# Kernel optimization log

Measured on AMD Instinct MI355X. Metric: run time of the kernel, lower is better.

Reference implementation:

```python
import jax, jax.numpy as jnp
import numpy as np

EPS_NORM = 1e-12  # torch F.normalize eps
EPS_SUM = 1e-8
NEG_BIG = -1e9    # mask value for softmax (sims/temp is bounded by 10)


def setup_inputs() -> dict:
    key = jax.random.key(0)
    k1, k2 = jax.random.split(key)
    B, R, D = 128, 4096, 256
    reps = jax.random.normal(k1, (B, R, D), dtype=jnp.float32)
    query_rels = jax.random.randint(k2, (B,), 0, R, dtype=jnp.int64)
    # learned scalar params (per __init__ defaults: thr_init=0.8, strength_init=0.05)
    threshold_raw = jnp.asarray(0.8 * 2.0 - 1.0, dtype=jnp.float32)
    strength_raw = jnp.asarray(0.05 * 5.0 - 1.0, dtype=jnp.float32)
    weight_scale = jnp.asarray(1.0, dtype=jnp.float32)
    temperature = jnp.asarray(1.0, dtype=jnp.float32)
    return {
        "final_relation_representations": reps,
        "query_rels": query_rels,
        "threshold_raw": threshold_raw,
        "strength_raw": strength_raw,
        "weight_scale": weight_scale,
        "temperature": temperature,
    }


def reference(final_relation_representations, query_rels, threshold_raw,
              strength_raw, weight_scale, temperature):
    threshold = jax.nn.sigmoid(threshold_raw)            # in (0,1)
    strength = jax.nn.sigmoid(strength_raw) * 0.2        # in (0,0.2)
    temp = jnp.clip(temperature, 0.1, 10.0)

    def per_sample(r, qidx):
        # r: [R, D], qidx: scalar int
        q = r[qidx]                                                   # [D]
        qn = q / jnp.maximum(jnp.linalg.norm(q), EPS_NORM)            # [D]
        an = r / jnp.maximum(jnp.linalg.norm(r, axis=1, keepdims=True), EPS_NORM)
        sims = an @ qn                                                # [R]
        sims = sims.at[qidx].set(-1.0)                                # exclude self
        sim_w = jax.nn.sigmoid((sims - threshold) * 10.0)             # smooth gate
        mask = sim_w > 0.5                                            # == sims > threshold
        maskf = mask.astype(r.dtype)
        # softmax over valid entries only (masked -> ~0 weight)
        logits = jnp.where(mask, sims / temp, NEG_BIG)
        w = jax.nn.softmax(logits)
        combined = w * sim_w * maskf
        adjusted = combined * (1.0 + weight_scale * sims)
        adjusted = adjusted / (adjusted.sum() + EPS_SUM)
        weighted = adjusted @ r                                       # [D]
        has_valid = mask.any()
        new_row = jnp.where(has_valid,
                            (1.0 - strength) * q + strength * weighted,
                            q)
        return r.at[qidx].set(new_row)

    return jax.vmap(per_sample)(final_relation_representations, query_rels)
```

## Files before the change

### kernel.cpp

```cpp
#include <hip/hip_runtime.h>
#include <math.h>

constexpr int R = 4096;
constexpr int D = 256;
constexpr int LOG2R = 12;

typedef float f32x4 __attribute__((ext_vector_type(4)));

__device__ __forceinline__ float wave_sum(float v) {
    #pragma unroll
    for (int o = 32; o >= 1; o >>= 1) v += __shfl_xor(v, o, 64);
    return v;
}

__global__ void knorm_q(const float* __restrict__ reps, const int* __restrict__ qrels,
                        float* __restrict__ qn) {
    int b = blockIdx.x;
    int qidx = qrels[b];
    const float* q = reps + ((size_t)b * R + (size_t)qidx) * D;
    int d = threadIdx.x;
    float v = q[d];
    float ss = wave_sum(v * v);
    __shared__ float red[4];
    int wave = threadIdx.x >> 6, lane = threadIdx.x & 63;
    if (lane == 0) red[wave] = ss;
    __syncthreads();
    float tot = red[0] + red[1] + red[2] + red[3];
    float nrm = fmaxf(sqrtf(tot), 1e-12f);
    qn[(size_t)b * D + d] = v / nrm;
}

__global__ void kcopy_sims(const float* __restrict__ reps, const float* __restrict__ qn,
                           float* __restrict__ out, float* __restrict__ sims) {
    int lane = threadIdx.x & 63;
    size_t wid = (size_t)blockIdx.x * 4 + (threadIdx.x >> 6);
    size_t nwaves = (size_t)gridDim.x * 4;
    const size_t total_rows = (size_t)128 * R;
    for (size_t row = wid; row < total_rows; row += nwaves) {
        int b = (int)(row >> LOG2R);
        const f32x4* src = (const f32x4*)(reps + row * D);
        f32x4 v = __builtin_nontemporal_load(src + lane);
        __builtin_nontemporal_store(v, (f32x4*)(out + row * D) + lane);
        f32x4 qv = ((const f32x4*)(qn + (size_t)b * D))[lane];
        float dot = v.x * qv.x + v.y * qv.y + v.z * qv.z + v.w * qv.w;
        float nrm = v.x * v.x + v.y * v.y + v.z * v.z + v.w * v.w;
        #pragma unroll
        for (int o = 32; o >= 1; o >>= 1) {
            dot += __shfl_xor(dot, o, 64);
            nrm += __shfl_xor(nrm, o, 64);
        }
        if (lane == 0) sims[row] = dot / fmaxf(sqrtf(nrm), 1e-12f);
    }
}

__global__ void kadjust_final(const float* __restrict__ reps, const float* __restrict__ sims,
                              const int* __restrict__ qrels,
                              const float* __restrict__ thrp, const float* __restrict__ strp,
                              const float* __restrict__ wsp, const float* __restrict__ tempp,
                              float* __restrict__ out) {
    __shared__ float s[R];
    __shared__ float redM[4], redS[4], redT[4];
    __shared__ int lidx[R];
    __shared__ float lco[R];
    __shared__ int nv_sh;
    int b = blockIdx.x;
    int qidx = qrels[b];
    const float* srow = sims + (size_t)b * R;
    for (int i = threadIdx.x; i < R; i += 256) s[i] = srow[i];
    if (threadIdx.x == 0) nv_sh = 0;
    __syncthreads();
    if (threadIdx.x == 0) s[qidx] = -1.0f;
    __syncthreads();

    float threshold = 1.f / (1.f + expf(-thrp[0]));
    float temp = fminf(fmaxf(tempp[0], 0.1f), 10.f);
    float wscale = wsp[0];
    int wave = threadIdx.x >> 6, lane = threadIdx.x & 63;

    float M = -1e9f;
    for (int i = threadIdx.x; i < R; i += 256) {
        float sv = s[i];
        if (sv > threshold) M = fmaxf(M, sv / temp);
    }
    #pragma unroll
    for (int o = 32; o >= 1; o >>= 1) M = fmaxf(M, __shfl_xor(M, o, 64));
    if (lane == 0) redM[wave] = M;
    __syncthreads();
    M = fmaxf(fmaxf(redM[0], redM[1]), fmaxf(redM[2], redM[3]));

    float S = 0.f, T = 0.f;
    for (int i = threadIdx.x; i < R; i += 256) {
        float sv = s[i];
        bool m = sv > threshold;
        float logit = m ? sv / temp : -1e9f;
        float e = expf(logit - M);
        float g = 0.f;
        if (m) {
            float simw = 1.f / (1.f + expf(-(sv - threshold) * 10.f));
            g = simw * (1.f + wscale * sv);
        }
        S += e; T += e * g;
    }
    S = wave_sum(S); T = wave_sum(T);
    if (lane == 0) { redS[wave] = S; redT[wave] = T; }
    __syncthreads();
    S = redS[0] + redS[1] + redS[2] + redS[3];
    T = redT[0] + redT[1] + redT[2] + redT[3];
    float denom = T + 1e-8f * S;

    for (int i = threadIdx.x; i < R; i += 256) {
        float sv = s[i];
        if (sv > threshold) {
            float e = expf(sv / temp - M);
            float simw = 1.f / (1.f + expf(-(sv - threshold) * 10.f));
            float a = e * simw * (1.f + wscale * sv) / denom;
            int p = atomicAdd(&nv_sh, 1);
            lidx[p] = i;
            lco[p] = a;
        }
    }
    __syncthreads();
    int nv = nv_sh;
    if (nv == 0) return;

    int d = threadIdx.x;
    const float* rb = reps + (size_t)b * R * D;
    float acc = 0.f;
    for (int j = 0; j < nv; j++)
        acc += lco[j] * rb[(size_t)lidx[j] * D + d];
    float strength = (1.f / (1.f + expf(-strp[0]))) * 0.2f;
    float qd = rb[(size_t)qidx * D + d];
    out[((size_t)b * R + (size_t)qidx) * D + d] = (1.f - strength) * qd + strength * acc;
}

extern "C" void kernel_launch(void* const* d_in, const int* in_sizes, int n_in,
                              void* d_out, int out_size, void* d_ws, size_t ws_size,
                              hipStream_t stream) {
    const float* reps  = (const float*)d_in[0];
    const int*   qrels = (const int*)d_in[1];
    const float* thrp  = (const float*)d_in[2];
    const float* strp  = (const float*)d_in[3];
    const float* wsp   = (const float*)d_in[4];
    const float* tempp = (const float*)d_in[5];
    float* out = (float*)d_out;
    int B = in_sizes[1];

    float* qn   = (float*)d_ws;
    float* sims = qn + (size_t)B * D;

    knorm_q      <<<B,    256, 0, stream>>>(reps, qrels, qn);
    kcopy_sims   <<<2048, 256, 0, stream>>>(reps, qn, out, sims);
    kadjust_final<<<B,    256, 0, stream>>>(reps, sims, qrels, thrp, strp, wsp, tempp, out);
}
```

Before: 869.3 us.

## Process four rows per wave in copy-sims kernel with 16-lane reductions

```diff
diff --git a/kernel.cpp b/kernel.cpp
--- a/kernel.cpp
+++ b/kernel.cpp
@@ -32,24 +32,46 @@
 
 __global__ void kcopy_sims(const float* __restrict__ reps, const float* __restrict__ qn,
                            float* __restrict__ out, float* __restrict__ sims) {
-    int lane = threadIdx.x & 63;
-    size_t wid = (size_t)blockIdx.x * 4 + (threadIdx.x >> 6);
+    const int lane = threadIdx.x & 63;
+    const int sub  = lane >> 4;
+    const int l16  = lane & 15;
+    size_t wid    = (size_t)blockIdx.x * 4 + (threadIdx.x >> 6);
     size_t nwaves = (size_t)gridDim.x * 4;
-    const size_t total_rows = (size_t)128 * R;
-    for (size_t row = wid; row < total_rows; row += nwaves) {
+    const size_t ngroups = ((size_t)128 * R) / 4;
+    int bprev = -1;
+    f32x4 qv0, qv1, qv2, qv3;
+    for (size_t g = wid; g < ngroups; g += nwaves) {
+        size_t row = g * 4 + sub;
         int b = (int)(row >> LOG2R);
+        if (b != bprev) {
+            const f32x4* qp = (const f32x4*)(qn + (size_t)b * D);
+            qv0 = qp[l16]; qv1 = qp[l16 + 16]; qv2 = qp[l16 + 32]; qv3 = qp[l16 + 48];
+            bprev = b;
+        }
         const f32x4* src = (const f32x4*)(reps + row * D);
-        f32x4 v = __builtin_nontemporal_load(src + lane);
-        __builtin_nontemporal_store(v, (f32x4*)(out + row * D) + lane);
-        f32x4 qv = ((const f32x4*)(qn + (size_t)b * D))[lane];
-        float dot = v.x * qv.x + v.y * qv.y + v.z * qv.z + v.w * qv.w;
-        float nrm = v.x * v.x + v.y * v.y + v.z * v.z + v.w * v.w;
+        f32x4*       dst = (f32x4*)(out + row * D);
+        f32x4 v0 = __builtin_nontemporal_load(src + l16);
+        f32x4 v1 = __builtin_nontemporal_load(src + l16 + 16);
+        f32x4 v2 = __builtin_nontemporal_load(src + l16 + 32);
+        f32x4 v3 = __builtin_nontemporal_load(src + l16 + 48);
+        __builtin_nontemporal_store(v0, dst + l16);
+        __builtin_nontemporal_store(v1, dst + l16 + 16);
+        __builtin_nontemporal_store(v2, dst + l16 + 32);
+        __builtin_nontemporal_store(v3, dst + l16 + 48);
+        float dot = v0.x * qv0.x + v0.y * qv0.y + v0.z * qv0.z + v0.w * qv0.w
+                  + v1.x * qv1.x + v1.y * qv1.y + v1.z * qv1.z + v1.w * qv1.w
+                  + v2.x * qv2.x + v2.y * qv2.y + v2.z * qv2.z + v2.w * qv2.w
+                  + v3.x * qv3.x + v3.y * qv3.y + v3.z * qv3.z + v3.w * qv3.w;
+        float nrm = v0.x * v0.x + v0.y * v0.y + v0.z * v0.z + v0.w * v0.w
+                  + v1.x * v1.x + v1.y * v1.y + v1.z * v1.z + v1.w * v1.w
+                  + v2.x * v2.x + v2.y * v2.y + v2.z * v2.z + v2.w * v2.w
+                  + v3.x * v3.x + v3.y * v3.y + v3.z * v3.z + v3.w * v3.w;
         #pragma unroll
-        for (int o = 32; o >= 1; o >>= 1) {
+        for (int o = 8; o >= 1; o >>= 1) {
             dot += __shfl_xor(dot, o, 64);
             nrm += __shfl_xor(nrm, o, 64);
         }
-        if (lane == 0) sims[row] = dot / fmaxf(sqrtf(nrm), 1e-12f);
+        if (l16 == 0) sims[row] = dot / fmaxf(sqrtf(nrm), 1e-12f);
     }
 }
 
```

After: 836.2 us. 1.04x faster.
